# Kernel optimization log

Measured on AMD Instinct MI355X. Metric: run time of the kernel, lower is better.

## Reference

```python
import jax, jax.numpy as jnp
import numpy as np

EMBED_DIM = 1024
NUM_HEADS = 16
HEAD_DIM = EMBED_DIM // NUM_HEADS


def setup_inputs() -> dict:
    key = jax.random.key(0)
    ks = jax.random.split(key, 9)
    B, T, D = 4, 2048, EMBED_DIM
    s = 1.0 / np.sqrt(D)
    inp = {
        "x": jax.random.normal(ks[0], (B, T, D), dtype=jnp.float32),
        "Wq": jax.random.normal(ks[1], (D, D), dtype=jnp.float32) * s,
        "bq": jnp.zeros((D,), dtype=jnp.float32),
        "Wk": jax.random.normal(ks[2], (D, D), dtype=jnp.float32) * s,
        "bk": jnp.zeros((D,), dtype=jnp.float32),
        "Wv": jax.random.normal(ks[3], (D, D), dtype=jnp.float32) * s,
        "bv": jnp.zeros((D,), dtype=jnp.float32),
        "Wo": jax.random.normal(ks[4], (D, D), dtype=jnp.float32) * s,
        "bo": jnp.zeros((D,), dtype=jnp.float32),
    }
    return inp


def _attn(x, Wq, bq, Wk, bk, Wv, bv, Wo, bo):
    B, T, D = x.shape
    H, Hd = NUM_HEADS, HEAD_DIM
    # projections: Linear uses y = x @ W^T + b; here W stored as (D, D) acting as W^T already
    q = (x @ Wq + bq).reshape(B, T, H, Hd).transpose(0, 2, 1, 3)  # [B,H,T,Hd]
    k = (x @ Wk + bk).reshape(B, T, H, Hd).transpose(0, 2, 1, 3)
    v = (x @ Wv + bv).reshape(B, T, H, Hd).transpose(0, 2, 1, 3)
    scores = jnp.einsum("bhqd,bhkd->bhqk", q, k) / np.sqrt(Hd)  # [B,H,T,T]
    causal = jnp.tril(jnp.ones((T, T), dtype=bool))
    scores = jnp.where(causal, scores, -jnp.inf)
    w = jax.nn.softmax(scores, axis=-1)
    out = jnp.einsum("bhqk,bhkd->bhqd", w, v)  # [B,H,T,Hd]
    out = out.transpose(0, 2, 1, 3).reshape(B, T, D)
    return out @ Wo + bo


def reference(x, Wq, bq, Wk, bk, Wv, bv, Wo, bo):
    return _attn(x, Wq, bq, Wk, bk, Wv, bv, Wo, bo)
```

## Files before the change

kernel.cpp:

```cpp
#include <hip/hip_runtime.h>
#include <cstdint>
#include <cstddef>

#define DI __device__ __forceinline__

typedef unsigned short u16;
typedef short bf16x8 __attribute__((ext_vector_type(8)));
typedef unsigned short u16x8 __attribute__((ext_vector_type(8)));
typedef float f32x4 __attribute__((ext_vector_type(4)));

static constexpr int DMODEL = 1024, T = 2048, BB = 4, NH = 16, HD = 64;
static constexpr int M = BB * T;

static constexpr size_t XB_OFF = 0;
static constexpr size_t WT_OFF = (size_t)M * DMODEL;
static constexpr size_t Q_OFF  = WT_OFF + 4ull * DMODEL * DMODEL;
static constexpr size_t K_OFF  = Q_OFF + (size_t)M * DMODEL;
static constexpr size_t V_OFF  = K_OFF + (size_t)M * DMODEL;
static constexpr size_t O_OFF  = XB_OFF;

DI u16 f2bf(float x) {
  unsigned int u = __builtin_bit_cast(unsigned int, x);
  u += 0x7fffu + ((u >> 16) & 1u);
  return (u16)(u >> 16);
}

DI unsigned int cvtpk_bf16(float a, float b) {
  unsigned int r;
  asm("v_cvt_pk_bf16_f32 %0, %1, %2" : "=v"(r) : "v"(a), "v"(b));
  return r;
}

DI void gld_lds16(const void* g, void* l) {
  __builtin_amdgcn_global_load_lds(
      (const __attribute__((address_space(1))) void*)g,
      (__attribute__((address_space(3))) void*)l, 16, 0, 0);
}

__global__ void k_cast(const float* __restrict__ in, u16* __restrict__ out) {
  size_t i = (size_t)(blockIdx.x * 256 + threadIdx.x) * 8;
  float4 a = *(const float4*)(in + i);
  float4 b = *(const float4*)(in + i + 4);
  u16x8 v;
  v[0] = f2bf(a.x); v[1] = f2bf(a.y); v[2] = f2bf(a.z); v[3] = f2bf(a.w);
  v[4] = f2bf(b.x); v[5] = f2bf(b.y); v[6] = f2bf(b.z); v[7] = f2bf(b.w);
  *(u16x8*)(out + i) = v;
}

__global__ void k_transw(const float* __restrict__ Wq, const float* __restrict__ Wk,
                         const float* __restrict__ Wv, const float* __restrict__ Wo,
                         u16* __restrict__ WtBase) {
  __shared__ u16 tile[32][33];
  const int z = blockIdx.z;
  const float* W = z == 0 ? Wq : (z == 1 ? Wk : (z == 2 ? Wv : Wo));
  u16* Wt = WtBase + (size_t)z * DMODEL * DMODEL;
  int tx = threadIdx.x, ty = threadIdx.y;
  int c = blockIdx.x * 32 + tx;
#pragma unroll
  for (int i = 0; i < 4; ++i) {
    int r = blockIdx.y * 32 + ty + i * 8;
    tile[ty + i * 8][tx] = f2bf(W[(size_t)r * DMODEL + c]);
  }
  __syncthreads();
#pragma unroll
  for (int i = 0; i < 4; ++i) {
    int rw = blockIdx.x * 32 + ty + i * 8;
    Wt[(size_t)rw * DMODEL + blockIdx.y * 32 + tx] = tile[tx][ty + i * 8];
  }
}

__launch_bounds__(256, 2)
__global__ void k_gemm_qkv(const u16* __restrict__ A, const u16* __restrict__ Wt,
                           const float* __restrict__ bq, const float* __restrict__ bk,
                           const float* __restrict__ bv,
                           u16* __restrict__ Qo, u16* __restrict__ Ko, u16* __restrict__ Vo) {
  __shared__ u16 As[128 * 64];
  __shared__ u16 Bs[128 * 64];
  const int z = blockIdx.z;
  const u16* Bt = Wt + (size_t)z * DMODEL * DMODEL;
  const float* bias = z == 0 ? bq : (z == 1 ? bk : bv);
  u16* out = z == 0 ? Qo : (z == 1 ? Ko : Vo);
  const float scale = z == 0 ? 0.125f * 1.4426950408889634f : 1.0f;

  const int tid = threadIdx.x;
  const int wave = tid >> 6, lane = tid & 63;
  const int g = lane >> 4, l15 = lane & 15;
  const int brow = blockIdx.x * 128, bcol = blockIdx.y * 128;
  const int wr = wave >> 1, wc = wave & 1;
  const int srow = tid >> 3, schunk = tid & 7;

  f32x4 acc[4][4] = {};

  for (int k0 = 0; k0 < DMODEL; k0 += 64) {
    __syncthreads();
#pragma unroll
    for (int j = 0; j < 4; ++j) {
      int r = j * 32 + srow;
      int cs = (schunk ^ (r & 7)) * 8;
      gld_lds16(A + (size_t)(brow + r) * DMODEL + k0 + cs, (char*)As + j * 4096 + wave * 1024);
      gld_lds16(Bt + (size_t)(bcol + r) * DMODEL + k0 + cs, (char*)Bs + j * 4096 + wave * 1024);
    }
    __syncthreads();
#pragma unroll
    for (int kh = 0; kh < 2; ++kh) {
      bf16x8 af[4], bfr[4];
#pragma unroll
      for (int m = 0; m < 4; ++m) {
        int r = wr * 64 + m * 16 + l15;
        int ch = (kh * 4 + g) ^ (r & 7);
        af[m] = *(const bf16x8*)((const char*)As + r * 128 + ch * 16);
      }
#pragma unroll
      for (int n = 0; n < 4; ++n) {
        int r = wc * 64 + n * 16 + l15;
        int ch = (kh * 4 + g) ^ (r & 7);
        bfr[n] = *(const bf16x8*)((const char*)Bs + r * 128 + ch * 16);
      }
#pragma unroll
      for (int m = 0; m < 4; ++m)
#pragma unroll
        for (int n = 0; n < 4; ++n)
          acc[m][n] = __builtin_amdgcn_mfma_f32_16x16x32_bf16(af[m], bfr[n], acc[m][n], 0, 0, 0);
    }
  }

#pragma unroll
  for (int m = 0; m < 4; ++m)
#pragma unroll
    for (int n = 0; n < 4; ++n) {
      int col = bcol + wc * 64 + n * 16 + l15;
      float bias_v = bias[col];
      int h = col >> 6, d = col & 63;
#pragma unroll
      for (int r = 0; r < 4; ++r) {
        int row = brow + wr * 64 + m * 16 + g * 4 + r;
        int b = row >> 11, t = row & 2047;
        float v = (acc[m][n][r] + bias_v) * scale;
        out[(((size_t)(b * NH + h) * T + t) << 6) + d] = f2bf(v);
      }
    }
}

__launch_bounds__(256, 2)
__global__ void k_gemm_out(const u16* __restrict__ A, const u16* __restrict__ Bt,
                           const float* __restrict__ bias, float* __restrict__ out) {
  __shared__ u16 As[128 * 64];
  __shared__ u16 Bs[128 * 64];
  const int tid = threadIdx.x;
  const int wave = tid >> 6, lane = tid & 63;
  const int g = lane >> 4, l15 = lane & 15;
  const int brow = blockIdx.x * 128, bcol = blockIdx.y * 128;
  const int wr = wave >> 1, wc = wave & 1;
  const int srow = tid >> 3, schunk = tid & 7;

  f32x4 acc[4][4] = {};

  for (int k0 = 0; k0 < DMODEL; k0 += 64) {
    __syncthreads();
#pragma unroll
    for (int j = 0; j < 4; ++j) {
      int r = j * 32 + srow;
      int cs = (schunk ^ (r & 7)) * 8;
      gld_lds16(A + (size_t)(brow + r) * DMODEL + k0 + cs, (char*)As + j * 4096 + wave * 1024);
      gld_lds16(Bt + (size_t)(bcol + r) * DMODEL + k0 + cs, (char*)Bs + j * 4096 + wave * 1024);
    }
    __syncthreads();
#pragma unroll
    for (int kh = 0; kh < 2; ++kh) {
      bf16x8 af[4], bfr[4];
#pragma unroll
      for (int m = 0; m < 4; ++m) {
        int r = wr * 64 + m * 16 + l15;
        int ch = (kh * 4 + g) ^ (r & 7);
        af[m] = *(const bf16x8*)((const char*)As + r * 128 + ch * 16);
      }
#pragma unroll
      for (int n = 0; n < 4; ++n) {
        int r = wc * 64 + n * 16 + l15;
        int ch = (kh * 4 + g) ^ (r & 7);
        bfr[n] = *(const bf16x8*)((const char*)Bs + r * 128 + ch * 16);
      }
#pragma unroll
      for (int m = 0; m < 4; ++m)
#pragma unroll
        for (int n = 0; n < 4; ++n)
          acc[m][n] = __builtin_amdgcn_mfma_f32_16x16x32_bf16(af[m], bfr[n], acc[m][n], 0, 0, 0);
    }
  }

#pragma unroll
  for (int m = 0; m < 4; ++m)
#pragma unroll
    for (int n = 0; n < 4; ++n) {
      int col = bcol + wc * 64 + n * 16 + l15;
      float bias_v = bias[col];
#pragma unroll
      for (int r = 0; r < 4; ++r) {
        int row = brow + wr * 64 + m * 16 + g * 4 + r;
        out[(size_t)row * DMODEL + col] = acc[m][n][r] + bias_v;
      }
    }
}

__launch_bounds__(256, 4)
__global__ void k_attn(const u16* __restrict__ Qw, const u16* __restrict__ Kw,
                       const u16* __restrict__ Vw, u16* __restrict__ Ow) {
  __shared__ u16 Ks[2][64 * 64];
  __shared__ u16 Vt[2][64 * 64];
  __shared__ u16 Ot[64 * 64];

  const int tid = threadIdx.x;
  const int wave = tid >> 6, lane = tid & 63;
  const int g = lane >> 4, l15 = lane & 15;
  const int tl = (l15 & 3) | ((l15 & 4) << 1) | ((l15 & 8) >> 1);
  const int l = blockIdx.x;
  const int xcd = l & 7, w = l >> 3;
  const int bh = xcd + ((w & 7) << 3);
  const int qp = w >> 3;
  const u16* Qb = Qw + (size_t)bh * T * HD;
  const u16* Kb = Kw + (size_t)bh * T * HD;
  const u16* Vb = Vw + (size_t)bh * T * HD;
  const int b = bh >> 4, h = bh & 15;
  const int vp = tid & 31, vcg = tid >> 5;
  const int krow = tid >> 3, kchunk = tid & 7;

  for (int half = 0; half < 2; ++half) {
    const int qt = half == 0 ? (31 - qp) : qp;
    const int ntiles = qt + 1;

    bf16x8 qf[2];
    {
      int qrow = qt * 64 + wave * 16 + l15;
#pragma unroll
      for (int kh = 0; kh < 2; ++kh)
        qf[kh] = *(const bf16x8*)(Qb + (size_t)qrow * HD + kh * 32 + g * 8);
    }

    f32x4 oacc[4] = {};
    float mrun = -1e30f, lrun = 0.f;

    {
      const u16* gv = Vb + (size_t)(2 * vp) * HD + vcg * 8;
      bf16x8 v0 = *(const bf16x8*)gv;
      bf16x8 v1 = *(const bf16x8*)(gv + HD);
#pragma unroll
      for (int j = 0; j < 2; ++j) {
        int r = j * 32 + krow;
        gld_lds16(Kb + (size_t)r * HD + (kchunk ^ (r & 7)) * 8,
                  (char*)(Ks[0]) + j * 4096 + wave * 1024);
      }
      char* vtb = (char*)(Vt[0]);
      const unsigned int* w0 = (const unsigned int*)&v0;
      const unsigned int* w1 = (const unsigned int*)&v1;
#pragma unroll
      for (int d2 = 0; d2 < 4; ++d2) {
        int c0 = vcg * 8 + 2 * d2, c1 = c0 + 1;
        unsigned int pk0 = __builtin_amdgcn_perm(w1[d2], w0[d2], 0x05040100u);
        unsigned int pk1 = __builtin_amdgcn_perm(w1[d2], w0[d2], 0x07060302u);
        *(unsigned int*)(vtb + ((c0 * 128 + 4 * vp) ^ ((c0 & 7) << 4))) = pk0;
        *(unsigned int*)(vtb + ((c1 * 128 + 4 * vp) ^ ((c1 & 7) << 4))) = pk1;
      }
    }

    for (int kt = 0; kt < ntiles; ++kt) {
      __syncthreads();
      const int cur = kt & 1;
      const bool havenext = (kt + 1 < ntiles);

      bf16x8 v0, v1;
      if (havenext) {
        const u16* gv = Vb + (size_t)((kt + 1) * 64 + 2 * vp) * HD + vcg * 8;
        v0 = *(const bf16x8*)gv;
        v1 = *(const bf16x8*)(gv + HD);
#pragma unroll
        for (int j = 0; j < 2; ++j) {
          int r = j * 32 + krow;
          gld_lds16(Kb + (size_t)((kt + 1) * 64 + r) * HD + (kchunk ^ (r & 7)) * 8,
                    (char*)(Ks[cur ^ 1]) + j * 4096 + wave * 1024);
        }
      }

      bf16x8 kf[2][4];
#pragma unroll
      for (int kh = 0; kh < 2; ++kh)
#pragma unroll
        for (int n = 0; n < 4; ++n) {
          int rr = n * 16 + tl;
          int ch = (kh * 4 + g) ^ (rr & 7);
          kf[kh][n] = *(const bf16x8*)((const char*)(Ks[cur]) + rr * 128 + ch * 16);
        }

      f32x4 s[4] = {};
      __builtin_amdgcn_s_setprio(1);
#pragma unroll
      for (int kh = 0; kh < 2; ++kh)
#pragma unroll
        for (int n = 0; n < 4; ++n)
          s[n] = __builtin_amdgcn_mfma_f32_16x16x32_bf16(kf[kh][n], qf[kh], s[n], 0, 0, 0);
      __builtin_amdgcn_s_setprio(0);

      if (kt == qt) {
        int q_in = wave * 16 + l15;
#pragma unroll
        for (int n = 0; n < 4; ++n)
#pragma unroll
          for (int r = 0; r < 4; ++r) {
            int kv_in = n * 16 + (g & 1) * 8 + (g >> 1) * 4 + r;
            if (kv_in > q_in) s[n][r] = -1e30f;
          }
      }

      float t0 = fmaxf(fmaxf(s[0][0], s[0][1]), s[0][2]);
      float t1 = fmaxf(fmaxf(s[0][3], s[1][0]), s[1][1]);
      float t2 = fmaxf(fmaxf(s[1][2], s[1][3]), s[2][0]);
      float t3 = fmaxf(fmaxf(s[2][1], s[2][2]), s[2][3]);
      float t4 = fmaxf(fmaxf(s[3][0], s[3][1]), s[3][2]);
      float vmax = fmaxf(fmaxf(fmaxf(t0, t1), t2), fmaxf(fmaxf(t3, t4), s[3][3]));
      vmax = fmaxf(vmax, __shfl_xor(vmax, 16));
      vmax = fmaxf(vmax, __shfl_xor(vmax, 32));

      if (!__all(vmax - mrun <= 8.f)) {
        float mnew = fmaxf(mrun, vmax);
        float a = exp2f(mrun - mnew);
        lrun *= a;
#pragma unroll
        for (int n = 0; n < 4; ++n)
#pragma unroll
          for (int r = 0; r < 4; ++r) oacc[n][r] *= a;
        mrun = mnew;
      }

      float ps0 = 0.f, ps1 = 0.f, ps2 = 0.f, ps3 = 0.f;
#pragma unroll
      for (int n = 0; n < 4; ++n) {
        float p0 = exp2f(s[n][0] - mrun);
        float p1 = exp2f(s[n][1] - mrun);
        float p2 = exp2f(s[n][2] - mrun);
        float p3 = exp2f(s[n][3] - mrun);
        s[n][0] = p0; s[n][1] = p1; s[n][2] = p2; s[n][3] = p3;
        ps0 += p0; ps1 += p1; ps2 += p2; ps3 += p3;
      }
      lrun += (ps0 + ps1) + (ps2 + ps3);

      __builtin_amdgcn_s_setprio(1);
#pragma unroll
      for (int kvh = 0; kvh < 2; ++kvh) {
        const int nlo = kvh * 2, nhi = kvh * 2 + 1;
        unsigned int L0 = cvtpk_bf16(s[nlo][0], s[nlo][1]);
        unsigned int L1 = cvtpk_bf16(s[nlo][2], s[nlo][3]);
        unsigned int H0 = cvtpk_bf16(s[nhi][0], s[nhi][1]);
        unsigned int H1 = cvtpk_bf16(s[nhi][2], s[nhi][3]);
        asm volatile("v_permlane32_swap_b32 %0, %1" : "+v"(L0), "+v"(H0));
        asm volatile("v_permlane32_swap_b32 %0, %1" : "+v"(L1), "+v"(H1));
        bf16x8 pb;
        unsigned int* pw = (unsigned int*)&pb;
        pw[0] = L0; pw[1] = L1; pw[2] = H0; pw[3] = H1;

        const int ch = ((kvh * 4 + g) ^ (l15 & 7)) * 16;
#pragma unroll
        for (int n = 0; n < 4; ++n) {
          bf16x8 an = *(const bf16x8*)((const char*)(Vt[cur]) + (n * 16 + l15) * 128 + ch);
          oacc[n] = __builtin_amdgcn_mfma_f32_16x16x32_bf16(an, pb, oacc[n], 0, 0, 0);
        }
      }
      __builtin_amdgcn_s_setprio(0);

      if (havenext) {
        char* vtb = (char*)(Vt[cur ^ 1]);
        const unsigned int* w0 = (const unsigned int*)&v0;
        const unsigned int* w1 = (const unsigned int*)&v1;
#pragma unroll
        for (int d2 = 0; d2 < 4; ++d2) {
          int c0 = vcg * 8 + 2 * d2, c1 = c0 + 1;
          unsigned int pk0 = __builtin_amdgcn_perm(w1[d2], w0[d2], 0x05040100u);
          unsigned int pk1 = __builtin_amdgcn_perm(w1[d2], w0[d2], 0x07060302u);
          *(unsigned int*)(vtb + ((c0 * 128 + 4 * vp) ^ ((c0 & 7) << 4))) = pk0;
          *(unsigned int*)(vtb + ((c1 * 128 + 4 * vp) ^ ((c1 & 7) << 4))) = pk1;
        }
      }
    }

    {
      float ltot = lrun;
      ltot += __shfl_xor(ltot, 16);
      ltot += __shfl_xor(ltot, 32);
      float inv = 1.f / ltot;
      char* otb = (char*)Ot;
#pragma unroll
      for (int n = 0; n < 4; ++n)
#pragma unroll
        for (int i = 0; i < 2; ++i) {
          unsigned int w2 = cvtpk_bf16(oacc[n][2 * i] * inv, oacc[n][2 * i + 1] * inv);
          int didx = n * 8 + g * 2 + i;
          int off = (wave * 16 + l15) * 128 + ((didx * 4) ^ ((l15 & 7) << 4));
          *(unsigned int*)(otb + off) = w2;
        }
      __syncthreads();
      int q = tid >> 2, seg = tid & 3;
      uint4 c0 = *(const uint4*)(otb + q * 128 + (((seg * 2) ^ (q & 7)) << 4));
      uint4 c1 = *(const uint4*)(otb + q * 128 + (((seg * 2 + 1) ^ (q & 7)) << 4));
      u16* dst = Ow + ((size_t)b * T + qt * 64 + q) * DMODEL + h * 64 + seg * 16;
      *(uint4*)dst = c0;
      *(uint4*)(dst + 8) = c1;
    }
  }
}

extern "C" void kernel_launch(void* const* d_in, const int* in_sizes, int n_in,
                              void* d_out, int out_size, void* d_ws, size_t ws_size,
                              hipStream_t stream) {
  const float* x  = (const float*)d_in[0];
  const float* Wq = (const float*)d_in[1];
  const float* bq = (const float*)d_in[2];
  const float* Wk = (const float*)d_in[3];
  const float* bk = (const float*)d_in[4];
  const float* Wv = (const float*)d_in[5];
  const float* bv = (const float*)d_in[6];
  const float* Wo = (const float*)d_in[7];
  const float* bo = (const float*)d_in[8];
  float* out = (float*)d_out;
  u16* ws = (u16*)d_ws;

  k_cast<<<4096, 256, 0, stream>>>(x, ws + XB_OFF);
  k_transw<<<dim3(32, 32, 4), dim3(32, 8), 0, stream>>>(Wq, Wk, Wv, Wo, ws + WT_OFF);
  k_gemm_qkv<<<dim3(64, 8, 3), 256, 0, stream>>>(ws + XB_OFF, ws + WT_OFF, bq, bk, bv,
                                                 ws + Q_OFF, ws + K_OFF, ws + V_OFF);
  k_attn<<<1024, 256, 0, stream>>>(ws + Q_OFF, ws + K_OFF, ws + V_OFF, ws + O_OFF);
  k_gemm_out<<<dim3(64, 8), 256, 0, stream>>>(ws + O_OFF, ws + WT_OFF + 3ull * DMODEL * DMODEL,
                                              bo, out);
}
```

Before: 165.1 us.

## Write V pre-transposed from projection GEMM and load it asynchronously in attention

Splits the V projection into its own GEMM that writes V in a [b,h,d,t] layout, so the attention kernel can load V tiles into LDS with direct asynchronous global-to-LDS loads like K. This removes per-tile register staging, byte permutes and LDS stores for the V transpose in the attention inner loop. In exchange, the V GEMM epilogue does strided, poorly coalesced stores, and there is one extra kernel launch.

```diff
diff --git a/kernel.cpp b/kernel.cpp
--- a/kernel.cpp
+++ b/kernel.cpp
@@ -72,14 +72,13 @@
 __launch_bounds__(256, 2)
 __global__ void k_gemm_qkv(const u16* __restrict__ A, const u16* __restrict__ Wt,
                            const float* __restrict__ bq, const float* __restrict__ bk,
-                           const float* __restrict__ bv,
-                           u16* __restrict__ Qo, u16* __restrict__ Ko, u16* __restrict__ Vo) {
+                           u16* __restrict__ Qo, u16* __restrict__ Ko) {
   __shared__ u16 As[128 * 64];
   __shared__ u16 Bs[128 * 64];
   const int z = blockIdx.z;
   const u16* Bt = Wt + (size_t)z * DMODEL * DMODEL;
-  const float* bias = z == 0 ? bq : (z == 1 ? bk : bv);
-  u16* out = z == 0 ? Qo : (z == 1 ? Ko : Vo);
+  const float* bias = z == 0 ? bq : bk;
+  u16* out = z == 0 ? Qo : Ko;
   const float scale = z == 0 ? 0.125f * 1.4426950408889634f : 1.0f;
 
   const int tid = threadIdx.x;
@@ -139,6 +138,69 @@
         out[(((size_t)(b * NH + h) * T + t) << 6) + d] = f2bf(v);
       }
     }
+}
+
+__launch_bounds__(256, 2)
+__global__ void k_gemm_v(const u16* __restrict__ A, const u16* __restrict__ Bt,
+                         const float* __restrict__ bias, u16* __restrict__ VTo) {
+  __shared__ u16 As[128 * 64];
+  __shared__ u16 Bs[128 * 64];
+  const int tid = threadIdx.x;
+  const int wave = tid >> 6, lane = tid & 63;
+  const int g = lane >> 4, l15 = lane & 15;
+  const int brow = blockIdx.x * 128, bcol = blockIdx.y * 128;
+  const int wr = wave >> 1, wc = wave & 1;
+  const int srow = tid >> 3, schunk = tid & 7;
+
+  f32x4 acc[4][4] = {};
+
+  for (int k0 = 0; k0 < DMODEL; k0 += 64) {
+    __syncthreads();
+#pragma unroll
+    for (int j = 0; j < 4; ++j) {
+      int r = j * 32 + srow;
+      int cs = (schunk ^ (r & 7)) * 8;
+      gld_lds16(A + (size_t)(brow + r) * DMODEL + k0 + cs, (char*)As + j * 4096 + wave * 1024);
+      gld_lds16(Bt + (size_t)(bcol + r) * DMODEL + k0 + cs, (char*)Bs + j * 4096 + wave * 1024);
+    }
+    __syncthreads();
+#pragma unroll
+    for (int kh = 0; kh < 2; ++kh) {
+      bf16x8 af[4], bfr[4];
+#pragma unroll
+      for (int m = 0; m < 4; ++m) {
+        int r = wr * 64 + m * 16 + l15;
+        int ch = (kh * 4 + g) ^ (r & 7);
+        af[m] = *(const bf16x8*)((const char*)As + r * 128 + ch * 16);
+      }
+#pragma unroll
+      for (int n = 0; n < 4; ++n) {
+        int r = wc * 64 + n * 16 + l15;
+        int ch = (kh * 4 + g) ^ (r & 7);
+        bfr[n] = *(const bf16x8*)((const char*)Bs + r * 128 + ch * 16);
+      }
+#pragma unroll
+      for (int m = 0; m < 4; ++m)
+#pragma unroll
+        for (int n = 0; n < 4; ++n)
+          acc[m][n] = __builtin_amdgcn_mfma_f32_16x16x32_bf16(bfr[n], af[m], acc[m][n], 0, 0, 0);
+    }
+  }
+
+#pragma unroll
+  for (int m = 0; m < 4; ++m) {
+    int trow = brow + wr * 64 + m * 16 + l15;
+    int b = trow >> 11, t = trow & 2047;
+#pragma unroll
+    for (int n = 0; n < 4; ++n)
+#pragma unroll
+      for (int r = 0; r < 4; ++r) {
+        int dg = bcol + wc * 64 + n * 16 + g * 4 + r;
+        float v = acc[m][n][r] + bias[dg];
+        int h = dg >> 6, dd = dg & 63;
+        VTo[(((size_t)(b * NH + h)) * 64 + dd) * T + t] = f2bf(v);
+      }
+  }
 }
 
 __launch_bounds__(256, 2)
@@ -204,7 +266,7 @@
 
 __launch_bounds__(256, 4)
 __global__ void k_attn(const u16* __restrict__ Qw, const u16* __restrict__ Kw,
-                       const u16* __restrict__ Vw, u16* __restrict__ Ow) {
+                       const u16* __restrict__ VTw, u16* __restrict__ Ow) {
   __shared__ u16 Ks[2][64 * 64];
   __shared__ u16 Vt[2][64 * 64];
   __shared__ u16 Ot[64 * 64];
@@ -219,9 +281,8 @@
   const int qp = w >> 3;
   const u16* Qb = Qw + (size_t)bh * T * HD;
   const u16* Kb = Kw + (size_t)bh * T * HD;
-  const u16* Vb = Vw + (size_t)bh * T * HD;
+  const u16* Vb = VTw + (size_t)bh * HD * T;
   const int b = bh >> 4, h = bh & 15;
-  const int vp = tid & 31, vcg = tid >> 5;
   const int krow = tid >> 3, kchunk = tid & 7;
 
   for (int half = 0; half < 2; ++half) {
@@ -239,27 +300,13 @@
     f32x4 oacc[4] = {};
     float mrun = -1e30f, lrun = 0.f;
 
-    {
-      const u16* gv = Vb + (size_t)(2 * vp) * HD + vcg * 8;
-      bf16x8 v0 = *(const bf16x8*)gv;
-      bf16x8 v1 = *(const bf16x8*)(gv + HD);
-#pragma unroll
-      for (int j = 0; j < 2; ++j) {
-        int r = j * 32 + krow;
-        gld_lds16(Kb + (size_t)r * HD + (kchunk ^ (r & 7)) * 8,
-                  (char*)(Ks[0]) + j * 4096 + wave * 1024);
-      }
-      char* vtb = (char*)(Vt[0]);
-      const unsigned int* w0 = (const unsigned int*)&v0;
-      const unsigned int* w1 = (const unsigned int*)&v1;
-#pragma unroll
-      for (int d2 = 0; d2 < 4; ++d2) {
-        int c0 = vcg * 8 + 2 * d2, c1 = c0 + 1;
-        unsigned int pk0 = __builtin_amdgcn_perm(w1[d2], w0[d2], 0x05040100u);
-        unsigned int pk1 = __builtin_amdgcn_perm(w1[d2], w0[d2], 0x07060302u);
-        *(unsigned int*)(vtb + ((c0 * 128 + 4 * vp) ^ ((c0 & 7) << 4))) = pk0;
-        *(unsigned int*)(vtb + ((c1 * 128 + 4 * vp) ^ ((c1 & 7) << 4))) = pk1;
-      }
+#pragma unroll
+    for (int j = 0; j < 2; ++j) {
+      int r = j * 32 + krow;
+      gld_lds16(Kb + (size_t)r * HD + (kchunk ^ (r & 7)) * 8,
+                (char*)(Ks[0]) + j * 4096 + wave * 1024);
+      gld_lds16(Vb + (size_t)r * T + (kchunk ^ (r & 7)) * 8,
+                (char*)(Vt[0]) + j * 4096 + wave * 1024);
     }
 
     for (int kt = 0; kt < ntiles; ++kt) {
@@ -267,16 +314,14 @@
       const int cur = kt & 1;
       const bool havenext = (kt + 1 < ntiles);
 
-      bf16x8 v0, v1;
       if (havenext) {
-        const u16* gv = Vb + (size_t)((kt + 1) * 64 + 2 * vp) * HD + vcg * 8;
-        v0 = *(const bf16x8*)gv;
-        v1 = *(const bf16x8*)(gv + HD);
 #pragma unroll
         for (int j = 0; j < 2; ++j) {
           int r = j * 32 + krow;
           gld_lds16(Kb + (size_t)((kt + 1) * 64 + r) * HD + (kchunk ^ (r & 7)) * 8,
                     (char*)(Ks[cur ^ 1]) + j * 4096 + wave * 1024);
+          gld_lds16(Vb + (size_t)r * T + (kt + 1) * 64 + (kchunk ^ (r & 7)) * 8,
+                    (char*)(Vt[cur ^ 1]) + j * 4096 + wave * 1024);
         }
       }
 
@@ -364,20 +409,6 @@
         }
       }
       __builtin_amdgcn_s_setprio(0);
-
-      if (havenext) {
-        char* vtb = (char*)(Vt[cur ^ 1]);
-        const unsigned int* w0 = (const unsigned int*)&v0;
-        const unsigned int* w1 = (const unsigned int*)&v1;
-#pragma unroll
-        for (int d2 = 0; d2 < 4; ++d2) {
-          int c0 = vcg * 8 + 2 * d2, c1 = c0 + 1;
-          unsigned int pk0 = __builtin_amdgcn_perm(w1[d2], w0[d2], 0x05040100u);
-          unsigned int pk1 = __builtin_amdgcn_perm(w1[d2], w0[d2], 0x07060302u);
-          *(unsigned int*)(vtb + ((c0 * 128 + 4 * vp) ^ ((c0 & 7) << 4))) = pk0;
-          *(unsigned int*)(vtb + ((c1 * 128 + 4 * vp) ^ ((c1 & 7) << 4))) = pk1;
-        }
-      }
     }
 
     {
@@ -423,8 +454,10 @@
 
   k_cast<<<4096, 256, 0, stream>>>(x, ws + XB_OFF);
   k_transw<<<dim3(32, 32, 4), dim3(32, 8), 0, stream>>>(Wq, Wk, Wv, Wo, ws + WT_OFF);
-  k_gemm_qkv<<<dim3(64, 8, 3), 256, 0, stream>>>(ws + XB_OFF, ws + WT_OFF, bq, bk, bv,
-                                                 ws + Q_OFF, ws + K_OFF, ws + V_OFF);
+  k_gemm_qkv<<<dim3(64, 8, 2), 256, 0, stream>>>(ws + XB_OFF, ws + WT_OFF, bq, bk,
+                                                 ws + Q_OFF, ws + K_OFF);
+  k_gemm_v<<<dim3(64, 8), 256, 0, stream>>>(ws + XB_OFF, ws + WT_OFF + 2ull * DMODEL * DMODEL,
+                                            bv, ws + V_OFF);
   k_attn<<<1024, 256, 0, stream>>>(ws + Q_OFF, ws + K_OFF, ws + V_OFF, ws + O_OFF);
   k_gemm_out<<<dim3(64, 8), 256, 0, stream>>>(ws + O_OFF, ws + WT_OFF + 3ull * DMODEL * DMODEL,
                                               bo, out);
```

Result: no change. 167.2 us (+1.2%).
